# Kernel tuning notes

Hardware: AMD Instinct MI355X
Metric: run time of the kernel (lower is better)

## Reference

```python
import jax, jax.numpy as jnp
import numpy as np

S, B, I, H = 512, 64, 256, 512


def setup_inputs() -> dict:
    key = jax.random.key(0)
    ks = jax.random.split(key, 17)
    def lin(k, out_d, in_d):
        bound = 1.0 / np.sqrt(in_d)
        kw, kb = jax.random.split(k)
        W = jax.random.uniform(kw, (out_d, in_d), jnp.float32, -bound, bound)
        b = jax.random.uniform(kb, (out_d,), jnp.float32, -bound, bound)
        return W, b
    Wfi, bfi = lin(ks[1], H, I)
    Wfh, bfh = lin(ks[2], H, H)
    Wii, bii = lin(ks[3], H, I)
    Wih, bih = lin(ks[4], H, H)
    Wci, bci = lin(ks[5], H, I)
    Wch, bch = lin(ks[6], H, H)
    Woi, boi = lin(ks[7], H, I)
    Woh, boh = lin(ks[8], H, H)
    x = jax.random.normal(ks[0], (S, B, I), jnp.float32)
    h = jnp.zeros((1, B, H), jnp.float32)
    c = jnp.zeros((1, B, H), jnp.float32)
    return {"x": x, "h": h, "c": c,
            "Wfi": Wfi, "bfi": bfi, "Wfh": Wfh, "bfh": bfh,
            "Wii": Wii, "bii": bii, "Wih": Wih, "bih": bih,
            "Wci": Wci, "bci": bci, "Wch": Wch, "bch": bch,
            "Woi": Woi, "boi": boi, "Woh": Woh, "boh": boh}


def reference(x, h, c, Wfi, bfi, Wfh, bfh, Wii, bii, Wih, bih,
              Wci, bci, Wch, bch, Woi, boi, Woh, boh):
    # x: (S,B,I); h,c: (1,B,H). Faithful to original broadcasting semantics.
    def step(carry, xt):
        h, c = carry  # (1,B,H)
        f_t = jax.nn.sigmoid(xt @ Wfi.T + bfi + h @ Wfh.T + bfh)
        i_t = jax.nn.sigmoid(xt @ Wii.T + bii + h @ Wih.T + bih)
        ct_t = jnp.tanh(xt @ Wci.T + bci + h @ Wch.T + bch)
        c = c * f_t + i_t * ct_t
        o_t = jax.nn.sigmoid(xt @ Woi.T + boi + h @ Woh.T + boh)
        h = o_t * jnp.tanh(c)
        return (h, c), h[0]  # store squeezed (B,H)
    (h, c), h_seq = jax.lax.scan(step, (h, c), x)
    return h_seq, h, c
```

## Files before the change

kernel.cpp:

```cpp
#include <hip/hip_runtime.h>


#define SS 512
#define BB 64
#define II 256
#define HH 512
#define NWG 32
#define GROW 2048
#define TBN  (SS*BB)

typedef unsigned int u32;
typedef unsigned short u16;
typedef unsigned long long u64;
typedef _Float16 __attribute__((ext_vector_type(8))) h16x8;
typedef __attribute__((ext_vector_type(2))) float f32x2;
typedef __attribute__((ext_vector_type(4))) float f32x4;
typedef __attribute__((ext_vector_type(16))) float f32x16;
typedef u32 __attribute__((ext_vector_type(4))) u32x4;
typedef u32 __attribute__((ext_vector_type(2))) u32x2;

#define A2_DW   (8 * 8 * 2 * 16 * 256)
#define WXA_DW  (64 * 16 * 256)
#define XA2_OFF  0
#define XWXA_OFF ((size_t)A2_DW * 4)
#define XBS_OFF  (XWXA_OFF + (size_t)WXA_DW * 4)
#define XHB_OFF  (XBS_OFF + 8192)
#define XFL_OFF  (XHB_OFF + 2 * (size_t)BB * HH * 2)
#define XXP_OFF  ((size_t)4 * 1024 * 1024)
#define XP_BYTES ((size_t)GROW * TBN * 2)
#define WS_XP    (XXP_OFF + XP_BYTES)

#define A_DWORDS (32 * 2 * 2 * 24 * 64 * 4)
#define HB_OFF   ((size_t)A_DWORDS * 4)
#define FL_OFF   (HB_OFF + 2 * (size_t)BB * HH * 2)
#define WS_NEED  (FL_OFF + 4096)

__device__ __forceinline__ u32 pk2h(float a, float b) {
    union { _Float16 h[2]; u32 u; } v;
    v.h[0] = (_Float16)a; v.h[1] = (_Float16)b; return v.u;
}
__device__ __forceinline__ u16 f2h(float a) {
    union { _Float16 h; u16 u; } v; v.h = (_Float16)a; return v.u;
}
__device__ __forceinline__ float h2f(u16 u) {
    union { u16 u; _Float16 h; } v; v.u = u; return (float)v.h;
}
__device__ __forceinline__ float sigf(float v)  { return 1.0f / (1.0f + __expf(-v)); }
__device__ __forceinline__ float tanhf_(float v){ return 1.0f - 2.0f / (1.0f + __expf(2.0f * v)); }

__device__ __forceinline__ void st_u32_coh(u32* p, u32 v) {
    __hip_atomic_store(p, v, __ATOMIC_RELAXED, __HIP_MEMORY_SCOPE_AGENT);
}
__device__ __forceinline__ void st_u64_coh(u64* p, u64 v) {
    __hip_atomic_store(p, v, __ATOMIC_RELAXED, __HIP_MEMORY_SCOPE_AGENT);
}
__device__ __forceinline__ void st_i32_coh(int* p, int v) {
    __hip_atomic_store(p, v, __ATOMIC_RELAXED, __HIP_MEMORY_SCOPE_AGENT);
}
__device__ __forceinline__ int ld_i32_coh(const int* p) {
    return __hip_atomic_load(p, __ATOMIC_RELAXED, __HIP_MEMORY_SCOPE_AGENT);
}
__device__ __forceinline__ u64 ld_u64_coh(const u64* p) {
    return __hip_atomic_load(p, __ATOMIC_RELAXED, __HIP_MEMORY_SCOPE_AGENT);
}


__global__ __launch_bounds__(256) void xprep_pack(
    const float* __restrict__ Wfi, const float* __restrict__ Wfh,
    const float* __restrict__ Wii, const float* __restrict__ Wih,
    const float* __restrict__ Wci, const float* __restrict__ Wch,
    const float* __restrict__ Woi, const float* __restrict__ Woh,
    const float* __restrict__ bfi, const float* __restrict__ bfh,
    const float* __restrict__ bii, const float* __restrict__ bih,
    const float* __restrict__ bci, const float* __restrict__ bch,
    const float* __restrict__ boi, const float* __restrict__ boh,
    u32* __restrict__ A2, u32* __restrict__ WXA, float* __restrict__ bsum)
{
    int tid = blockIdx.x * 256 + threadIdx.x;
    if (tid < A2_DW) {
        int d = tid & 3, l = (tid >> 2) & 63, ks = (tid >> 8) & 15;
        int tile = (tid >> 12) & 1, mt = (tid >> 13) & 7, hg = tid >> 16;
        int row15 = l & 15;
        int ulocal = row15 >> 2, g = row15 & 3;
        int j = hg * 64 + mt * 8 + tile * 4 + ulocal;
        int k = ks * 32 + (l >> 4) * 8 + d * 2;
        const float* Wh = (g == 0) ? Wfh : (g == 1) ? Wih : (g == 2) ? Wch : Woh;
        A2[tid] = pk2h(Wh[j * HH + k], Wh[j * HH + k + 1]);
    } else if (tid < A2_DW + WXA_DW) {
        int t2 = tid - A2_DW;
        int d = t2 & 3, l = (t2 >> 2) & 63, kt = (t2 >> 8) & 15, gt = t2 >> 12;
        int r = l & 31, g = r & 3;
        int j = gt * 8 + (r >> 2);
        int k = kt * 16 + (l >> 5) * 8 + d * 2;
        const float* Wi = (g == 0) ? Wfi : (g == 1) ? Wii : (g == 2) ? Wci : Woi;
        WXA[t2] = pk2h(Wi[j * II + k], Wi[j * II + k + 1]);
    } else if (tid < A2_DW + WXA_DW + GROW) {
        int grow = tid - A2_DW - WXA_DW;
        int r = grow & 31, gt = grow >> 5;
        int g = r & 3, j = gt * 8 + (r >> 2);
        const float* bi = (g == 0) ? bfi : (g == 1) ? bii : (g == 2) ? bci : boi;
        const float* bh = (g == 0) ? bfh : (g == 1) ? bih : (g == 2) ? bch : boh;
        bsum[grow] = bi[j] + bh[j];
    }
}

__global__ __launch_bounds__(256) void xprep_hb(
    const float* __restrict__ h0, u16* __restrict__ hb, int* __restrict__ flags)
{
    int tid = blockIdx.x * 256 + threadIdx.x;
    if (tid < BB * HH) hb[tid] = f2h(h0[tid]);
    if (tid < NWG) flags[tid * 16] = 0;
}

__global__ __launch_bounds__(512, 1) void xproj(
    const float* __restrict__ x, const u32* __restrict__ WXA,
    const float* __restrict__ bsum, u64* __restrict__ XPq)
{
    const int wgid = blockIdx.x;
    const int tid = threadIdx.x, lane = tid & 63, w = tid >> 6;
    const int TB0 = wgid * 128;
    __shared__ __align__(16) u32 XB[32 * 128 * 4];

    #pragma unroll
    for (int it = 0; it < 16; ++it) {
        int c = it * 512 + tid;
        int m = c >> 6, ck = c & 63;
        f32x4 v = *(const f32x4*)(x + (size_t)(TB0 + m) * II + ck * 4);
        u32x2 p; p.x = pk2h(v.x, v.y); p.y = pk2h(v.z, v.w);
        *(u32x2*)(XB + ((ck >> 1) * 128 + m) * 4 + (ck & 1) * 2) = p;
    }
    __syncthreads();

    const int gtw = w & 3, nh = w >> 2;
    const int khi = lane >> 5;
    for (int nt = 0; nt < 2; ++nt) {
        const int col = nh * 64 + nt * 32 + (lane & 31);
        const int tb = TB0 + col;
        const int t_ = tb >> 6, b_ = tb & 63;
        h16x8 bfr[16];
        #pragma unroll
        for (int kt = 0; kt < 16; ++kt)
            bfr[kt] = *(const h16x8*)(XB + ((kt * 2 + khi) * 128 + col) * 4);
        for (int gti = 0; gti < 16; ++gti) {
            const int gt = gtw * 16 + gti;
            f32x16 acc;
            #pragma unroll
            for (int rg = 0; rg < 16; ++rg)
                acc[rg] = bsum[gt * 32 + (rg & 3) + 8 * (rg >> 2) + 4 * khi];
            const u32* ap = WXA + (size_t)(gt * 16) * 256 + lane * 4;
            #pragma unroll
            for (int kt = 0; kt < 16; ++kt) {
                h16x8 af = *(const h16x8*)(ap + kt * 256);
                acc = __builtin_amdgcn_mfma_f32_32x32x16_f16(af, bfr[kt], acc, 0, 0, 0);
            }
            #pragma unroll
            for (int q = 0; q < 4; ++q) {
                int j = gt * 8 + 2 * q + khi;
                union { u16 s[4]; u64 u; } pk;
                pk.s[0] = f2h(acc[4 * q + 0]);
                pk.s[1] = f2h(acc[4 * q + 1]);
                pk.s[2] = f2h(acc[4 * q + 2]);
                pk.s[3] = f2h(acc[4 * q + 3]);
                XPq[((size_t)j * 512 + t_) * 64 + b_] = pk.u;
            }
        }
    }
}

__global__ __launch_bounds__(512, 2) void lstm_rec(
    const float* __restrict__ c0,
    const u32* __restrict__ A2, u16* __restrict__ hb, int* __restrict__ flags,
    const u64* __restrict__ XPq, float* __restrict__ out)
{
    const int wg = blockIdx.x;
    const int hg = wg >> 2, bg = wg & 3;
    const int tid = threadIdx.x, lane = tid & 63, mt = tid >> 6;
    const int bl = lane & 15;
    const int kq = lane >> 4;
    const int b  = bg * 16 + bl;

    __shared__ __align__(16) u16 HL[64 * 16 * 8];
    __shared__ __align__(16) u16 hst[16 * 64];
    u64* hb64  = (u64*)hb;
    u64* hst64 = (u64*)hst;
    char* HLc  = (char*)HL;

    h16x8 afr0[16], afr1[16];
    {
        const u32* a0 = A2 + ((size_t)((hg * 8 + mt) * 2 + 0) * 16) * 256 + lane * 4;
        const u32* a1 = A2 + ((size_t)((hg * 8 + mt) * 2 + 1) * 16) * 256 + lane * 4;
        #pragma unroll
        for (int ks = 0; ks < 16; ++ks) {
            afr0[ks] = *(const h16x8*)(a0 + ks * 256);
            afr1[ks] = *(const h16x8*)(a1 + ks * 256);
        }
    }

    const int j0 = hg * 64 + mt * 8 + kq;
    const int j1 = j0 + 4;

    float cst0 = c0[b * HH + j0];
    float cst1 = c0[b * HH + j1];

    for (int t = 0; t < SS; ++t) {
        u64 xq0 = XPq[((size_t)j0 * SS + t) * BB + b];
        u64 xq1 = XPq[((size_t)j1 * SS + t) * BB + b];

        if (tid < 8) { while (ld_i32_coh(&flags[(bg * 8 + tid) * 16]) < t) {} }
        asm volatile("" ::: "memory");
        __syncthreads();

        {
            const u64* src = hb64 + (size_t)(t & 1) * 8192 + bg * 2048;
            u64 v0 = ld_u64_coh(src + 0 * 512 + tid);
            u64 v1 = ld_u64_coh(src + 1 * 512 + tid);
            u64 v2 = ld_u64_coh(src + 2 * 512 + tid);
            u64 v3 = ld_u64_coh(src + 3 * 512 + tid);
            #pragma unroll
            for (int i = 0; i < 4; ++i) {
                u64 v = (i == 0) ? v0 : (i == 1) ? v1 : (i == 2) ? v2 : v3;
                int idx = i * 512 + tid;
                int blr = idx >> 7, k4 = idx & 127;
                int k8 = k4 >> 1, half = k4 & 1;
                *(u64*)(HLc + (k8 * 16 + (blr ^ (k8 & 7))) * 16 + half * 8) = v;
            }
        }
        __syncthreads();

        f32x4 acc0 = {0.f, 0.f, 0.f, 0.f}, acc1 = {0.f, 0.f, 0.f, 0.f};
        #pragma unroll
        for (int ks = 0; ks < 16; ++ks) {
            const int k8 = ks * 4 + kq;
            h16x8 bf = *(const h16x8*)(HLc + (k8 * 16 + (bl ^ (k8 & 7))) * 16);
            acc0 = __builtin_amdgcn_mfma_f32_16x16x32_f16(afr0[ks], bf, acc0, 0, 0, 0);
            acc1 = __builtin_amdgcn_mfma_f32_16x16x32_f16(afr1[ks], bf, acc1, 0, 0, 0);
        }

        float hv0, hv1;
        {
            union { u64 u; u16 s[4]; } xu; xu.u = xq0;
            float af = acc0[0] + h2f(xu.s[0]);
            float ai = acc0[1] + h2f(xu.s[1]);
            float ac = acc0[2] + h2f(xu.s[2]);
            float ao = acc0[3] + h2f(xu.s[3]);
            float cn = cst0 * sigf(af) + sigf(ai) * tanhf_(ac);
            cst0 = cn; hv0 = sigf(ao) * tanhf_(cn);
        }
        {
            union { u64 u; u16 s[4]; } xu; xu.u = xq1;
            float af = acc1[0] + h2f(xu.s[0]);
            float ai = acc1[1] + h2f(xu.s[1]);
            float ac = acc1[2] + h2f(xu.s[2]);
            float ao = acc1[3] + h2f(xu.s[3]);
            float cn = cst1 * sigf(af) + sigf(ai) * tanhf_(ac);
            cst1 = cn; hv1 = sigf(ao) * tanhf_(cn);
        }
        hst[bl * 64 + ((mt * 8 + kq)     ^ ((bl & 7) << 3))] = f2h(hv0);
        hst[bl * 64 + ((mt * 8 + 4 + kq) ^ ((bl & 7) << 3))] = f2h(hv1);

        if (t < SS - 1) {
            __syncthreads();
            if (tid < 256) {
                int blr = tid >> 4, ju = tid & 15;
                int sj = ((((ju >> 1) ^ (blr & 7)) << 1) | (ju & 1));
                st_u64_coh(hb64 + (size_t)((t + 1) & 1) * 8192 + bg * 2048
                               + blr * 128 + hg * 16 + ju,
                           hst64[blr * 16 + sj]);
            }
            __syncthreads();
            if (tid == 0) st_i32_coh(&flags[(bg * 8 + hg) * 16], t + 1);
        }

        out[((size_t)t * BB + b) * HH + j0] = hv0;
        out[((size_t)t * BB + b) * HH + j1] = hv1;
        if (t == SS - 1) {
            out[(size_t)SS * BB * HH + b * HH + j0] = hv0;
            out[(size_t)SS * BB * HH + b * HH + j1] = hv1;
            out[(size_t)SS * BB * HH + BB * HH + b * HH + j0] = cst0;
            out[(size_t)SS * BB * HH + BB * HH + b * HH + j1] = cst1;
        }
    }
}

__global__ __launch_bounds__(256) void prep_A(
    const float* __restrict__ Wfi, const float* __restrict__ Wfh,
    const float* __restrict__ Wii, const float* __restrict__ Wih,
    const float* __restrict__ Wci, const float* __restrict__ Wch,
    const float* __restrict__ Woi, const float* __restrict__ Woh,
    u32* __restrict__ A)
{
    int tid = blockIdx.x * 256 + threadIdx.x;
    int wg = tid / 24576;  int r = tid - wg * 24576;
    int mt = r / 12288;    r -= mt * 12288;
    int ks = r / 6144;     r -= ks * 6144;
    int kt = r / 256;      r -= kt * 256;
    int l  = r >> 2;       int d = r & 3;

    int row = mt * 32 + (l & 31);
    int g   = row >> 4;
    int j   = wg * 16 + (row & 15);
    int k   = ks * 384 + kt * 16 + (l >> 5) * 8 + d * 2;

    const float* Wi = (g == 0) ? Wfi : (g == 1) ? Wii : (g == 2) ? Wci : Woi;
    const float* Wh = (g == 0) ? Wfh : (g == 1) ? Wih : (g == 2) ? Wch : Woh;
    float w0, w1;
    if (k < II) { w0 = Wi[j * II + k];        w1 = Wi[j * II + k + 1]; }
    else        { int kk = k - II; w0 = Wh[j * HH + kk]; w1 = Wh[j * HH + kk + 1]; }
    A[tid] = pk2h(w0, w1);
}

__global__ __launch_bounds__(256) void prep_misc(
    const float* __restrict__ h0, u16* __restrict__ hb, int* __restrict__ flags)
{
    int tid = blockIdx.x * 256 + threadIdx.x;
    if (tid < BB * HH) {
        int b = tid >> 9, j = tid & 511;
        hb[(j >> 3) * 512 + b * 8 + (j & 7)] = f2h(h0[tid]);
    }
    if (tid < 32) flags[tid * 32] = 0;
}

__global__ __launch_bounds__(512, 1) void lstm_mfma(
    const float* __restrict__ x,  const float* __restrict__ c0,
    const float* __restrict__ bfi, const float* __restrict__ bfh,
    const float* __restrict__ bii, const float* __restrict__ bih,
    const float* __restrict__ bci, const float* __restrict__ bch,
    const float* __restrict__ boi, const float* __restrict__ boh,
    const u32* __restrict__ A, u16* __restrict__ hb, int* __restrict__ flags,
    float* __restrict__ out)
{
    const int wg   = blockIdx.x;
    const int tid  = threadIdx.x;
    const int lane = tid & 63;
    const int w    = tid >> 6;
    const int mt   = w & 1;
    const int nt2  = (w >> 1) & 1;
    const int ks   = w >> 2;
    const int khi  = lane >> 5;
    const int nb   = nt2 * 32 + (lane & 31);

    __shared__ __align__(16) u16 BS[8192 * 8];
    char* BSc = (char*)BS;

    h16x8 afr[24];
    {
        const u32* ab = A + ((wg * 2 + mt) * 2 + ks) * (24 * 256) + lane * 4;
        #pragma unroll
        for (int kt = 0; kt < 24; ++kt)
            afr[kt] = *(const h16x8*)(ab + kt * 256);
    }

    f32x16 acc_init;
    #pragma unroll
    for (int rg = 0; rg < 16; ++rg) {
        int row = mt * 32 + (rg & 3) + 8 * (rg >> 2) + 4 * khi;
        float bv = 0.0f;
        if (ks == 0) {
            int g = row >> 4, j = wg * 16 + (row & 15);
            const float* bi = (g == 0) ? bfi : (g == 1) ? bii : (g == 2) ? bci : boi;
            const float* bh = (g == 0) ? bfh : (g == 1) ? bih : (g == 2) ? bch : boh;
            bv = bi[j] + bh[j];
        }
        acc_init[rg] = bv;
    }

    const int bown = tid & 63;
    const int w8   = tid >> 6;
    const int j0   = wg * 16 + 2 * w8;
    float cst[2];
    {
        const f32x2 cv = *(const f32x2*)(c0 + bown * HH + j0);
        cst[0] = cv.x; cst[1] = cv.y;
    }

    #pragma unroll
    for (int i = 0; i < 4; ++i) {
        int cid = i * 512 + tid;
        int bq = cid >> 5, k8 = cid & 31;
        const f32x4* sp = (const f32x4*)(x + bq * II + k8 * 8);
        f32x4 v0 = sp[0], v1 = sp[1];
        u32x4 pk;
        pk.x = pk2h(v0[0], v0[1]); pk.y = pk2h(v0[2], v0[3]);
        pk.z = pk2h(v1[0], v1[1]); pk.w = pk2h(v1[2], v1[3]);
        *(u32x4*)&BSc[(k8 * 64 + (bq ^ (k8 & 7))) * 16] = pk;
    }

    for (int t = 0; t < SS; ++t) {
        const int cur = t & 1;
        float* GLp = (float*)(BSc + (size_t)(cur ^ 1) * 2048 * 16);

        {
            const u16* hsrc = hb + cur * (BB * HH);
            u64 hr[16];
            #pragma unroll
            for (int it = 0; it < 8; ++it) {
                int cd = it * 512 + tid;
                int k8h = cd >> 6, bpos = cd & 63;
                int bq = bpos ^ (k8h & 7);
                const u64* p = (const u64*)(hsrc + k8h * 512 + bq * 8);
                hr[2 * it]     = ld_u64_coh(p);
                hr[2 * it + 1] = ld_u64_coh(p + 1);
            }
            #pragma unroll
            for (int it = 0; it < 8; ++it) {
                int cd = it * 512 + tid;
                union { u64 q[2]; u32x4 v; } u;
                u.q[0] = hr[2 * it]; u.q[1] = hr[2 * it + 1];
                *(u32x4*)&BSc[(4096 + cd) * 16] = u.v;
            }
        }

        f32x4 xv[8];
        if (t + 1 < SS) {
            const float* xt = x + (size_t)(t + 1) * BB * II;
            #pragma unroll
            for (int i = 0; i < 4; ++i) {
                int cid = i * 512 + tid;
                int bq = cid >> 5, k8 = cid & 31;
                const f32x4* sp = (const f32x4*)(xt + bq * II + k8 * 8);
                xv[2 * i] = sp[0]; xv[2 * i + 1] = sp[1];
            }
        }

        __syncthreads();

        f32x16 acc = acc_init;
        #pragma unroll
        for (int kt = 0; kt < 24; ++kt) {
            int k8g = ks * 48 + kt * 2 + khi;
            int off;
            if (k8g < 32) { int q = k8g & 7;
                off = (cur * 2048 + k8g * 64 + ((nb ^ q))) * 16;
            } else {        int k8h = k8g - 32; int q = k8h & 7;
                off = (4096 + k8h * 64 + ((nb ^ q))) * 16;
            }
            h16x8 bf = *(const h16x8*)(BSc + off);
            acc = __builtin_amdgcn_mfma_f32_32x32x16_f16(afr[kt], bf, acc, 0, 0, 0);
        }

        #pragma unroll
        for (int rg = 0; rg < 16; ++rg) {
            int row = mt * 32 + (rg & 3) + 8 * (rg >> 2) + 4 * khi;
            GLp[ks * 4096 + row * 64 + nb] = acc[rg];
        }
        __syncthreads();

        float hv2[2];
        #pragma unroll
        for (int i = 0; i < 2; ++i) {
            int m = 2 * w8 + i;
            float af = GLp[(0 * 16 + m) * 64 + bown] + GLp[4096 + (0 * 16 + m) * 64 + bown];
            float ai = GLp[(1 * 16 + m) * 64 + bown] + GLp[4096 + (1 * 16 + m) * 64 + bown];
            float ac = GLp[(2 * 16 + m) * 64 + bown] + GLp[4096 + (2 * 16 + m) * 64 + bown];
            float ao = GLp[(3 * 16 + m) * 64 + bown] + GLp[4096 + (3 * 16 + m) * 64 + bown];
            float fg = sigf(af), ig = sigf(ai), cg = tanhf_(ac), og = sigf(ao);
            float cn = cst[i] * fg + ig * cg;
            cst[i] = cn;
            hv2[i] = og * tanhf_(cn);
        }
        {
            f32x2 ho; ho.x = hv2[0]; ho.y = hv2[1];
            *(f32x2*)(out + ((size_t)t * BB + bown) * HH + j0) = ho;
        }
        st_u32_coh((u32*)(hb + ((t + 1) & 1) * (BB * HH) + (j0 >> 3) * 512 + bown * 8 + (j0 & 7)),
                   pk2h(hv2[0], hv2[1]));

        if (t == SS - 1) {
            f32x2 ho; ho.x = hv2[0]; ho.y = hv2[1];
            f32x2 co; co.x = cst[0]; co.y = cst[1];
            *(f32x2*)(out + (size_t)SS * BB * HH + bown * HH + j0) = ho;
            *(f32x2*)(out + (size_t)SS * BB * HH + BB * HH + bown * HH + j0) = co;
            break;
        }

        __syncthreads();
        if (tid == 0) st_i32_coh(&flags[wg * 32], t + 1);

        #pragma unroll
        for (int i = 0; i < 4; ++i) {
            int cid = i * 512 + tid;
            int bq = cid >> 5, k8 = cid & 31;
            f32x4 v0 = xv[2 * i], v1 = xv[2 * i + 1];
            u32x4 pk;
            pk.x = pk2h(v0[0], v0[1]); pk.y = pk2h(v0[2], v0[3]);
            pk.z = pk2h(v1[0], v1[1]); pk.w = pk2h(v1[2], v1[3]);
            *(u32x4*)&BSc[((cur ^ 1) * 2048 + k8 * 64 + (bq ^ (k8 & 7))) * 16] = pk;
        }

        if (tid < 32) {
            while (ld_i32_coh(&flags[tid * 32]) < t + 1) {}
        }
        asm volatile("" ::: "memory");
        __syncthreads();
    }
}

extern "C" void kernel_launch(void* const* d_in, const int* in_sizes, int n_in,
                              void* d_out, int out_size, void* d_ws, size_t ws_size,
                              hipStream_t stream) {
    const float* x   = (const float*)d_in[0];
    const float* h0  = (const float*)d_in[1];
    const float* c0  = (const float*)d_in[2];
    const float* Wfi = (const float*)d_in[3];
    const float* bfi = (const float*)d_in[4];
    const float* Wfh = (const float*)d_in[5];
    const float* bfh = (const float*)d_in[6];
    const float* Wii = (const float*)d_in[7];
    const float* bii = (const float*)d_in[8];
    const float* Wih = (const float*)d_in[9];
    const float* bih = (const float*)d_in[10];
    const float* Wci = (const float*)d_in[11];
    const float* bci = (const float*)d_in[12];
    const float* Wch = (const float*)d_in[13];
    const float* bch = (const float*)d_in[14];
    const float* Woi = (const float*)d_in[15];
    const float* boi = (const float*)d_in[16];
    const float* Woh = (const float*)d_in[17];
    const float* boh = (const float*)d_in[18];

    if (ws_size >= WS_XP) {
        u32*   A2   = (u32*)((char*)d_ws + XA2_OFF);
        u32*   WXA  = (u32*)((char*)d_ws + XWXA_OFF);
        float* bsum = (float*)((char*)d_ws + XBS_OFF);
        u16*   hbb  = (u16*)((char*)d_ws + XHB_OFF);
        int*   flg  = (int*)((char*)d_ws + XFL_OFF);
        u64*   XPq  = (u64*)((char*)d_ws + XXP_OFF);

        xprep_pack<<<dim3((A2_DW + WXA_DW + GROW + 255) / 256), dim3(256), 0, stream>>>(
            Wfi, Wfh, Wii, Wih, Wci, Wch, Woi, Woh,
            bfi, bfh, bii, bih, bci, bch, boi, boh, A2, WXA, bsum);
        xprep_hb<<<dim3(128), dim3(256), 0, stream>>>(h0, hbb, flg);
        xproj<<<dim3(TBN / 128), dim3(512), 0, stream>>>(x, WXA, bsum, XPq);
        lstm_rec<<<dim3(NWG), dim3(512), 0, stream>>>(c0, A2, hbb, flg, XPq, (float*)d_out);
    } else {
        u32* A     = (u32*)d_ws;
        u16* hbb   = (u16*)((char*)d_ws + HB_OFF);
        int* flags = (int*)((char*)d_ws + FL_OFF);
        prep_A<<<dim3(A_DWORDS / 256), dim3(256), 0, stream>>>(
            Wfi, Wfh, Wii, Wih, Wci, Wch, Woi, Woh, A);
        prep_misc<<<dim3(128), dim3(256), 0, stream>>>(h0, hbb, flags);
        lstm_mfma<<<dim3(32), dim3(512), 0, stream>>>(
            x, c0, bfi, bfh, bii, bih, bci, bch, boi, boh,
            A, hbb, flags, (float*)d_out);
    }
}
```

Baseline: 1.398 ms.

## Replace flag-based step sync with tagged hidden-state messages polled directly

Drops the per-workgroup flag counters and the spin-wait plus barriers around them. Each fp16 hidden value is now packed with a 16-bit timestep tag into a 32-bit word, and consumers poll the exchange buffer until every tag matches the current step, so the data load doubles as the readiness check. This removes a flag round-trip and two barriers from each step of the serial recurrence. In exchange the exchanged buffer doubles in size, and output stores become coalesced paired writes taken from the shared staging buffer.

```diff
diff --git a/kernel.cpp b/kernel.cpp
--- a/kernel.cpp
+++ b/kernel.cpp
@@ -24,8 +24,7 @@
 #define XA2_OFF  0
 #define XWXA_OFF ((size_t)A2_DW * 4)
 #define XBS_OFF  (XWXA_OFF + (size_t)WXA_DW * 4)
-#define XHB_OFF  (XBS_OFF + 8192)
-#define XFL_OFF  (XHB_OFF + 2 * (size_t)BB * HH * 2)
+#define XMB_OFF  (XBS_OFF + 8192)
 #define XXP_OFF  ((size_t)4 * 1024 * 1024)
 #define XP_BYTES ((size_t)GROW * TBN * 2)
 #define WS_XP    (XXP_OFF + XP_BYTES)
@@ -104,12 +103,22 @@
     }
 }
 
-__global__ __launch_bounds__(256) void xprep_hb(
-    const float* __restrict__ h0, u16* __restrict__ hb, int* __restrict__ flags)
+__global__ __launch_bounds__(256) void xprep_mb(
+    const float* __restrict__ h0, u64* __restrict__ MB64)
 {
     int tid = blockIdx.x * 256 + threadIdx.x;
-    if (tid < BB * HH) hb[tid] = f2h(h0[tid]);
-    if (tid < NWG) flags[tid * 16] = 0;
+    int slot = tid >> 14, rem = tid & 16383;
+    int bg = rem >> 12, bl = (rem >> 8) & 15, kp = rem & 255;
+    int b = bg * 16 + bl;
+    u64 v;
+    if (slot == 0) {
+        u32 lo = ((u32)f2h(h0[b * HH + 2 * kp])     << 16);
+        u32 hi = ((u32)f2h(h0[b * HH + 2 * kp + 1]) << 16);
+        v = ((u64)hi << 32) | lo;
+    } else {
+        v = 0x0000FFFF0000FFFFull;
+    }
+    MB64[tid] = v;
 }
 
 __global__ __launch_bounds__(512, 1) void xproj(
@@ -169,7 +178,7 @@
 
 __global__ __launch_bounds__(512, 2) void lstm_rec(
     const float* __restrict__ c0,
-    const u32* __restrict__ A2, u16* __restrict__ hb, int* __restrict__ flags,
+    const u32* __restrict__ A2, u64* __restrict__ MB64,
     const u64* __restrict__ XPq, float* __restrict__ out)
 {
     const int wg = blockIdx.x;
@@ -180,10 +189,8 @@
     const int b  = bg * 16 + bl;
 
     __shared__ __align__(16) u16 HL[64 * 16 * 8];
-    __shared__ __align__(16) u16 hst[16 * 64];
-    u64* hb64  = (u64*)hb;
-    u64* hst64 = (u64*)hst;
-    char* HLc  = (char*)HL;
+    __shared__ __align__(16) u32 hst32[16 * 66];
+    char* HLc = (char*)HL;
 
     h16x8 afr0[16], afr1[16];
     {
@@ -203,27 +210,39 @@
     float cst1 = c0[b * HH + j1];
 
     for (int t = 0; t < SS; ++t) {
+        const u32 tagv = (u32)t;
+        const u64* src = MB64 + (size_t)(t & 1) * 16384 + bg * 4096;
+
+        u64 v[8];
+        #pragma unroll
+        for (int i = 0; i < 8; ++i) v[i] = ld_u64_coh(src + i * 512 + tid);
+
         u64 xq0 = XPq[((size_t)j0 * SS + t) * BB + b];
         u64 xq1 = XPq[((size_t)j1 * SS + t) * BB + b];
 
-        if (tid < 8) { while (ld_i32_coh(&flags[(bg * 8 + tid) * 16]) < t) {} }
-        asm volatile("" ::: "memory");
-        __syncthreads();
-
         {
-            const u64* src = hb64 + (size_t)(t & 1) * 8192 + bg * 2048;
-            u64 v0 = ld_u64_coh(src + 0 * 512 + tid);
-            u64 v1 = ld_u64_coh(src + 1 * 512 + tid);
-            u64 v2 = ld_u64_coh(src + 2 * 512 + tid);
-            u64 v3 = ld_u64_coh(src + 3 * 512 + tid);
-            #pragma unroll
-            for (int i = 0; i < 4; ++i) {
-                u64 v = (i == 0) ? v0 : (i == 1) ? v1 : (i == 2) ? v2 : v3;
-                int idx = i * 512 + tid;
-                int blr = idx >> 7, k4 = idx & 127;
-                int k8 = k4 >> 1, half = k4 & 1;
-                *(u64*)(HLc + (k8 * 16 + (blr ^ (k8 & 7))) * 16 + half * 8) = v;
-            }
+            bool ok;
+            do {
+                ok = true;
+                #pragma unroll
+                for (int i = 0; i < 8; ++i) {
+                    u32 lo = (u32)v[i], hi = (u32)(v[i] >> 32);
+                    ok = ok && ((lo & 0xFFFFu) == tagv) && ((hi & 0xFFFFu) == tagv);
+                }
+                if (ok) break;
+                #pragma unroll
+                for (int i = 0; i < 8; ++i) v[i] = ld_u64_coh(src + i * 512 + tid);
+            } while (true);
+        }
+
+        #pragma unroll
+        for (int i = 0; i < 8; ++i) {
+            int idx2 = i * 512 + tid;
+            int blr = idx2 >> 8, kp = idx2 & 255;
+            int k8 = kp >> 2, q = kp & 3;
+            u32 lo = (u32)v[i], hi = (u32)(v[i] >> 32);
+            u32 pk = (lo >> 16) | (hi & 0xFFFF0000u);
+            *(u32*)(HLc + (k8 * 16 + (blr ^ (k8 & 7))) * 16 + q * 4) = pk;
         }
         __syncthreads();
 
@@ -255,27 +274,30 @@
             float cn = cst1 * sigf(af) + sigf(ai) * tanhf_(ac);
             cst1 = cn; hv1 = sigf(ao) * tanhf_(cn);
         }
-        hst[bl * 64 + ((mt * 8 + kq)     ^ ((bl & 7) << 3))] = f2h(hv0);
-        hst[bl * 64 + ((mt * 8 + 4 + kq) ^ ((bl & 7) << 3))] = f2h(hv1);
-
-        if (t < SS - 1) {
-            __syncthreads();
-            if (tid < 256) {
-                int blr = tid >> 4, ju = tid & 15;
-                int sj = ((((ju >> 1) ^ (blr & 7)) << 1) | (ju & 1));
-                st_u64_coh(hb64 + (size_t)((t + 1) & 1) * 8192 + bg * 2048
-                               + blr * 128 + hg * 16 + ju,
-                           hst64[blr * 16 + sj]);
-            }
-            __syncthreads();
-            if (tid == 0) st_i32_coh(&flags[(bg * 8 + hg) * 16], t + 1);
-        }
-
-        out[((size_t)t * BB + b) * HH + j0] = hv0;
-        out[((size_t)t * BB + b) * HH + j1] = hv1;
+
+        const u32 tagn = (u32)(t + 1) & 0xFFFFu;
+        hst32[bl * 66 + (mt * 8 + kq)]     = ((u32)f2h(hv0) << 16) | tagn;
+        hst32[bl * 66 + (mt * 8 + 4 + kq)] = ((u32)f2h(hv1) << 16) | tagn;
+        __syncthreads();
+
+        {
+            const int br = tid >> 5, ju = tid & 31;
+            u64 pv = *(const u64*)(hst32 + br * 66 + 2 * ju);
+            if (t < SS - 1) {
+                st_u64_coh(MB64 + (size_t)((t + 1) & 1) * 16384 + bg * 4096
+                                + br * 256 + hg * 32 + ju, pv);
+            }
+            u32 lo = (u32)pv, hi = (u32)(pv >> 32);
+            f32x2 ho;
+            ho.x = h2f((u16)(lo >> 16));
+            ho.y = h2f((u16)(hi >> 16));
+            *(f32x2*)(out + ((size_t)t * BB + bg * 16 + br) * HH + hg * 64 + 2 * ju) = ho;
+            if (t == SS - 1) {
+                *(f32x2*)(out + (size_t)SS * BB * HH
+                              + (size_t)(bg * 16 + br) * HH + hg * 64 + 2 * ju) = ho;
+            }
+        }
         if (t == SS - 1) {
-            out[(size_t)SS * BB * HH + b * HH + j0] = hv0;
-            out[(size_t)SS * BB * HH + b * HH + j1] = hv1;
             out[(size_t)SS * BB * HH + BB * HH + b * HH + j0] = cst0;
             out[(size_t)SS * BB * HH + BB * HH + b * HH + j1] = cst1;
         }
@@ -522,16 +544,15 @@
         u32*   A2   = (u32*)((char*)d_ws + XA2_OFF);
         u32*   WXA  = (u32*)((char*)d_ws + XWXA_OFF);
         float* bsum = (float*)((char*)d_ws + XBS_OFF);
-        u16*   hbb  = (u16*)((char*)d_ws + XHB_OFF);
-        int*   flg  = (int*)((char*)d_ws + XFL_OFF);
+        u64*   MB64 = (u64*)((char*)d_ws + XMB_OFF);
         u64*   XPq  = (u64*)((char*)d_ws + XXP_OFF);
 
         xprep_pack<<<dim3((A2_DW + WXA_DW + GROW + 255) / 256), dim3(256), 0, stream>>>(
             Wfi, Wfh, Wii, Wih, Wci, Wch, Woi, Woh,
             bfi, bfh, bii, bih, bci, bch, boi, boh, A2, WXA, bsum);
-        xprep_hb<<<dim3(128), dim3(256), 0, stream>>>(h0, hbb, flg);
+        xprep_mb<<<dim3(128), dim3(256), 0, stream>>>(h0, MB64);
         xproj<<<dim3(TBN / 128), dim3(512), 0, stream>>>(x, WXA, bsum, XPq);
-        lstm_rec<<<dim3(NWG), dim3(512), 0, stream>>>(c0, A2, hbb, flg, XPq, (float*)d_out);
+        lstm_rec<<<dim3(NWG), dim3(512), 0, stream>>>(c0, A2, MB64, XPq, (float*)d_out);
     } else {
         u32* A     = (u32*)d_ws;
         u16* hbb   = (u16*)((char*)d_ws + HB_OFF);
```

After: 1.447 ms. +3.5%, slower.

## Replace flag barrier with tagged h mailbox and spread recurrence over 64 WGs

Applied to the files above, without the earlier changes.

Removes the per-step flag polling and the extra syncthreads/store phases. Each step's h value is packed with a 16-bit step tag into a u32 mailbox, so consumers poll the data itself with L2-scope (sc0) loads and fall back to agent-coherent loads from a shadow copy after many tries. The recurrent kernel now runs on 64 workgroups of 8 batch columns each instead of 32 of 16, which doubles parallelism but wastes half of each MFMA's B columns. This adds a dependence on L2 coherence across CUs (XCD/L2 partitioning on MI355X could make the fast path stale) and doubles mailbox traffic.

```diff
diff --git a/kernel.cpp b/kernel.cpp
--- a/kernel.cpp
+++ b/kernel.cpp
@@ -5,9 +5,9 @@
 #define BB 64
 #define II 256
 #define HH 512
-#define NWG 32
 #define GROW 2048
 #define TBN  (SS*BB)
+#define FAST_TRIES 1024
 
 typedef unsigned int u32;
 typedef unsigned short u16;
@@ -24,8 +24,8 @@
 #define XA2_OFF  0
 #define XWXA_OFF ((size_t)A2_DW * 4)
 #define XBS_OFF  (XWXA_OFF + (size_t)WXA_DW * 4)
-#define XHB_OFF  (XBS_OFF + 8192)
-#define XFL_OFF  (XHB_OFF + 2 * (size_t)BB * HH * 2)
+#define XMBF_OFF (XBS_OFF + 8192)
+#define XMBS_OFF (XMBF_OFF + 262144)
 #define XXP_OFF  ((size_t)4 * 1024 * 1024)
 #define XP_BYTES ((size_t)GROW * TBN * 2)
 #define WS_XP    (XXP_OFF + XP_BYTES)
@@ -51,9 +51,6 @@
 __device__ __forceinline__ void st_u32_coh(u32* p, u32 v) {
     __hip_atomic_store(p, v, __ATOMIC_RELAXED, __HIP_MEMORY_SCOPE_AGENT);
 }
-__device__ __forceinline__ void st_u64_coh(u64* p, u64 v) {
-    __hip_atomic_store(p, v, __ATOMIC_RELAXED, __HIP_MEMORY_SCOPE_AGENT);
-}
 __device__ __forceinline__ void st_i32_coh(int* p, int v) {
     __hip_atomic_store(p, v, __ATOMIC_RELAXED, __HIP_MEMORY_SCOPE_AGENT);
 }
@@ -62,6 +59,23 @@
 }
 __device__ __forceinline__ u64 ld_u64_coh(const u64* p) {
     return __hip_atomic_load(p, __ATOMIC_RELAXED, __HIP_MEMORY_SCOPE_AGENT);
+}
+
+__device__ __forceinline__ void st_u32_l2(u32* p, u32 v) {
+    asm volatile("global_store_dword %0, %1, off sc0" :: "v"(p), "v"(v) : "memory");
+}
+__device__ __forceinline__ void ld4_u64_l2(const u64* p0, const u64* p1,
+                                           const u64* p2, const u64* p3,
+                                           u64& a, u64& b, u64& c, u64& d) {
+    asm volatile(
+        "global_load_dwordx2 %0, %4, off sc0\n\t"
+        "global_load_dwordx2 %1, %5, off sc0\n\t"
+        "global_load_dwordx2 %2, %6, off sc0\n\t"
+        "global_load_dwordx2 %3, %7, off sc0\n\t"
+        "s_waitcnt vmcnt(0)"
+        : "=&v"(a), "=&v"(b), "=&v"(c), "=&v"(d)
+        : "v"(p0), "v"(p1), "v"(p2), "v"(p3)
+        : "memory");
 }
 
 
@@ -104,12 +118,15 @@
     }
 }
 
-__global__ __launch_bounds__(256) void xprep_hb(
-    const float* __restrict__ h0, u16* __restrict__ hb, int* __restrict__ flags)
+__global__ __launch_bounds__(256) void xprep_mb2(
+    const float* __restrict__ h0, u32* __restrict__ MBF, u32* __restrict__ MBS)
 {
     int tid = blockIdx.x * 256 + threadIdx.x;
-    if (tid < BB * HH) hb[tid] = f2h(h0[tid]);
-    if (tid < NWG) flags[tid * 16] = 0;
+    int slot = tid >> 15, rem = tid & 32767;
+    int b = rem >> 9, j = rem & 511;
+    u32 v = (slot == 0) ? (((u32)f2h(h0[b * HH + j])) << 16) : 0x0000FFFFu;
+    MBF[tid] = v;
+    MBS[tid] = v;
 }
 
 __global__ __launch_bounds__(512, 1) void xproj(
@@ -167,23 +184,27 @@
     }
 }
 
-__global__ __launch_bounds__(512, 2) void lstm_rec(
+__global__ __launch_bounds__(512, 1) void lstm_rec(
     const float* __restrict__ c0,
-    const u32* __restrict__ A2, u16* __restrict__ hb, int* __restrict__ flags,
+    const u32* __restrict__ A2, u32* __restrict__ MBF, u32* __restrict__ MBS,
     const u64* __restrict__ XPq, float* __restrict__ out)
 {
-    const int wg = blockIdx.x;
-    const int hg = wg >> 2, bg = wg & 3;
+    const int bg = blockIdx.x & 7;
+    const int hg = blockIdx.x >> 3;
     const int tid = threadIdx.x, lane = tid & 63, mt = tid >> 6;
-    const int bl = lane & 15;
-    const int kq = lane >> 4;
-    const int b  = bg * 16 + bl;
+    const int col = lane & 15;
+    const int kq  = lane >> 4;
+    const int bc  = (col < 8) ? col : 7;
+    const int b   = bg * 8 + bc;
 
     __shared__ __align__(16) u16 HL[64 * 16 * 8];
-    __shared__ __align__(16) u16 hst[16 * 64];
-    u64* hb64  = (u64*)hb;
-    u64* hst64 = (u64*)hst;
-    char* HLc  = (char*)HL;
+    __shared__ __align__(16) u32 hst32[8 * 65];
+    char* HLc = (char*)HL;
+
+    for (int i = tid; i < 2048; i += 512) {
+        int r = i >> 5, rem = i & 31, c = 8 + (rem >> 2), q = rem & 3;
+        *(u32*)(HLc + (r * 16 + c) * 16 + q * 4) = 0;
+    }
 
     h16x8 afr0[16], afr1[16];
     {
@@ -202,28 +223,45 @@
     float cst0 = c0[b * HH + j0];
     float cst1 = c0[b * HH + j1];
 
+    bool slowmode = false;
+
     for (int t = 0; t < SS; ++t) {
         u64 xq0 = XPq[((size_t)j0 * SS + t) * BB + b];
         u64 xq1 = XPq[((size_t)j1 * SS + t) * BB + b];
 
-        if (tid < 8) { while (ld_i32_coh(&flags[(bg * 8 + tid) * 16]) < t) {} }
-        asm volatile("" ::: "memory");
-        __syncthreads();
-
-        {
-            const u64* src = hb64 + (size_t)(t & 1) * 8192 + bg * 2048;
-            u64 v0 = ld_u64_coh(src + 0 * 512 + tid);
-            u64 v1 = ld_u64_coh(src + 1 * 512 + tid);
-            u64 v2 = ld_u64_coh(src + 2 * 512 + tid);
-            u64 v3 = ld_u64_coh(src + 3 * 512 + tid);
-            #pragma unroll
-            for (int i = 0; i < 4; ++i) {
-                u64 v = (i == 0) ? v0 : (i == 1) ? v1 : (i == 2) ? v2 : v3;
-                int idx = i * 512 + tid;
-                int blr = idx >> 7, k4 = idx & 127;
-                int k8 = k4 >> 1, half = k4 & 1;
-                *(u64*)(HLc + (k8 * 16 + (blr ^ (k8 & 7))) * 16 + half * 8) = v;
-            }
+        const size_t g64 = (size_t)(t & 1) * 16384 + bg * 2048;
+        const u64* f64 = (const u64*)MBF + g64;
+        const u64* s64 = (const u64*)MBS + g64;
+        const u32 tg = (u32)t & 0xFFFFu;
+        u64 v0, v1, v2, v3;
+        int tries = 0;
+        for (;;) {
+            if (!slowmode) {
+                ld4_u64_l2(f64 + tid, f64 + 512 + tid, f64 + 1024 + tid, f64 + 1536 + tid,
+                           v0, v1, v2, v3);
+            } else {
+                v0 = ld_u64_coh(s64 + tid);
+                v1 = ld_u64_coh(s64 + 512 + tid);
+                v2 = ld_u64_coh(s64 + 1024 + tid);
+                v3 = ld_u64_coh(s64 + 1536 + tid);
+            }
+            bool ok = ((u32)v0 & 0xFFFFu) == tg && ((u32)(v0 >> 32) & 0xFFFFu) == tg
+                   && ((u32)v1 & 0xFFFFu) == tg && ((u32)(v1 >> 32) & 0xFFFFu) == tg
+                   && ((u32)v2 & 0xFFFFu) == tg && ((u32)(v2 >> 32) & 0xFFFFu) == tg
+                   && ((u32)v3 & 0xFFFFu) == tg && ((u32)(v3 >> 32) & 0xFFFFu) == tg;
+            if (ok) break;
+            if (!slowmode && ++tries > FAST_TRIES) slowmode = true;
+        }
+
+        #pragma unroll
+        for (int i = 0; i < 4; ++i) {
+            u64 v = (i == 0) ? v0 : (i == 1) ? v1 : (i == 2) ? v2 : v3;
+            int idx = i * 512 + tid;
+            int br = idx >> 8, jp = idx & 255;
+            int k8 = jp >> 2, q = jp & 3;
+            u32 lo = (u32)v, hi = (u32)(v >> 32);
+            u32 pk = (lo >> 16) | (hi & 0xFFFF0000u);
+            *(u32*)(HLc + (k8 * 16 + (br ^ (k8 & 7))) * 16 + q * 4) = pk;
         }
         __syncthreads();
 
@@ -231,7 +269,7 @@
         #pragma unroll
         for (int ks = 0; ks < 16; ++ks) {
             const int k8 = ks * 4 + kq;
-            h16x8 bf = *(const h16x8*)(HLc + (k8 * 16 + (bl ^ (k8 & 7))) * 16);
+            h16x8 bf = *(const h16x8*)(HLc + (k8 * 16 + (col ^ (k8 & 7))) * 16);
             acc0 = __builtin_amdgcn_mfma_f32_16x16x32_f16(afr0[ks], bf, acc0, 0, 0, 0);
             acc1 = __builtin_amdgcn_mfma_f32_16x16x32_f16(afr1[ks], bf, acc1, 0, 0, 0);
         }
@@ -255,27 +293,30 @@
             float cn = cst1 * sigf(af) + sigf(ai) * tanhf_(ac);
             cst1 = cn; hv1 = sigf(ao) * tanhf_(cn);
         }
-        hst[bl * 64 + ((mt * 8 + kq)     ^ ((bl & 7) << 3))] = f2h(hv0);
-        hst[bl * 64 + ((mt * 8 + 4 + kq) ^ ((bl & 7) << 3))] = f2h(hv1);
-
-        if (t < SS - 1) {
-            __syncthreads();
-            if (tid < 256) {
-                int blr = tid >> 4, ju = tid & 15;
-                int sj = ((((ju >> 1) ^ (blr & 7)) << 1) | (ju & 1));
-                st_u64_coh(hb64 + (size_t)((t + 1) & 1) * 8192 + bg * 2048
-                               + blr * 128 + hg * 16 + ju,
-                           hst64[blr * 16 + sj]);
-            }
-            __syncthreads();
-            if (tid == 0) st_i32_coh(&flags[(bg * 8 + hg) * 16], t + 1);
-        }
-
-        out[((size_t)t * BB + b) * HH + j0] = hv0;
-        out[((size_t)t * BB + b) * HH + j1] = hv1;
-        if (t == SS - 1) {
-            out[(size_t)SS * BB * HH + b * HH + j0] = hv0;
-            out[(size_t)SS * BB * HH + b * HH + j1] = hv1;
+
+        const u32 tagn = (u32)(t + 1) & 0xFFFFu;
+        if (col < 8) {
+            hst32[col * 65 + (mt * 8 + kq)]     = ((u32)f2h(hv0) << 16) | tagn;
+            hst32[col * 65 + (mt * 8 + 4 + kq)] = ((u32)f2h(hv1) << 16) | tagn;
+        }
+        __syncthreads();
+
+        {
+            const int br = tid >> 6, jl = tid & 63;
+            u32 pv = hst32[br * 65 + jl];
+            if (t < SS - 1) {
+                size_t pidx = (size_t)((t + 1) & 1) * 32768 + bg * 4096
+                            + br * 512 + hg * 64 + jl;
+                st_u32_l2(MBF + pidx, pv);
+                st_u32_coh(MBS + pidx, pv);
+            }
+            float ho = h2f((u16)(pv >> 16));
+            out[((size_t)t * BB + bg * 8 + br) * HH + hg * 64 + jl] = ho;
+            if (t == SS - 1) {
+                out[(size_t)SS * BB * HH + (size_t)(bg * 8 + br) * HH + hg * 64 + jl] = ho;
+            }
+        }
+        if (t == SS - 1 && col < 8) {
             out[(size_t)SS * BB * HH + BB * HH + b * HH + j0] = cst0;
             out[(size_t)SS * BB * HH + BB * HH + b * HH + j1] = cst1;
         }
@@ -522,16 +563,16 @@
         u32*   A2   = (u32*)((char*)d_ws + XA2_OFF);
         u32*   WXA  = (u32*)((char*)d_ws + XWXA_OFF);
         float* bsum = (float*)((char*)d_ws + XBS_OFF);
-        u16*   hbb  = (u16*)((char*)d_ws + XHB_OFF);
-        int*   flg  = (int*)((char*)d_ws + XFL_OFF);
+        u32*   MBF  = (u32*)((char*)d_ws + XMBF_OFF);
+        u32*   MBS  = (u32*)((char*)d_ws + XMBS_OFF);
         u64*   XPq  = (u64*)((char*)d_ws + XXP_OFF);
 
         xprep_pack<<<dim3((A2_DW + WXA_DW + GROW + 255) / 256), dim3(256), 0, stream>>>(
             Wfi, Wfh, Wii, Wih, Wci, Wch, Woi, Woh,
             bfi, bfh, bii, bih, bci, bch, boi, boh, A2, WXA, bsum);
-        xprep_hb<<<dim3(128), dim3(256), 0, stream>>>(h0, hbb, flg);
+        xprep_mb2<<<dim3(256), dim3(256), 0, stream>>>(h0, MBF, MBS);
         xproj<<<dim3(TBN / 128), dim3(512), 0, stream>>>(x, WXA, bsum, XPq);
-        lstm_rec<<<dim3(NWG), dim3(512), 0, stream>>>(c0, A2, hbb, flg, XPq, (float*)d_out);
+        lstm_rec<<<dim3(64), dim3(512), 0, stream>>>(c0, A2, MBF, MBS, XPq, (float*)d_out);
     } else {
         u32* A     = (u32*)d_ws;
         u16* hbb   = (u16*)((char*)d_ws + HB_OFF);
```

Result: slower. 5.585 ms (+299.4%).
